# Performance work log

Measured on AMD Instinct MI355X. Metric: run time of the kernel, lower is better.

Reference implementation:

```python
import jax, jax.numpy as jnp
import numpy as np

C = 256; G = 16; GC = C // G; K = 3; P = K * K
N = 4; H = 64; W = 64
PAD = 1; OFFSET_SCALE = 1.0; LN_EPS = 1e-5


def setup_inputs() -> dict:
    key = jax.random.key(0)
    ks = jax.random.split(key, 8)
    s = 0.02
    return {
        "x": jax.random.normal(ks[0], (N, C, H, W), jnp.float32),
        "dw_w": jax.random.normal(ks[1], (C, 1, K, K), jnp.float32) * s,
        "dw_b": jnp.zeros((C,), jnp.float32),
        "ln_g": jnp.ones((C,), jnp.float32),
        "ln_b": jnp.zeros((C,), jnp.float32),
        "off_w": jax.random.normal(ks[2], (C, G * P * 2), jnp.float32) * s,
        "off_b": jnp.zeros((G * P * 2,), jnp.float32),
        "mask_w": jax.random.normal(ks[3], (C, G * P), jnp.float32) * s,
        "mask_b": jnp.zeros((G * P,), jnp.float32),
        "inp_w": jax.random.normal(ks[4], (C, C), jnp.float32) * s,
        "inp_b": jnp.zeros((C,), jnp.float32),
        "out_w": jax.random.normal(ks[5], (C, C), jnp.float32) * s,
        "out_b": jnp.zeros((C,), jnp.float32),
    }


def _dcnv3_nchw(x, dw_w, dw_b, ln_g, ln_b, off_w, off_b, mask_w, mask_b,
                inp_w, inp_b, out_w, out_b):
    # NCHW -> NHWC (wrapper permute)
    xn = jnp.transpose(x, (0, 2, 3, 1))                      # (N,H,W,C)
    x_proj = xn @ inp_w + inp_b                              # input_proj

    # offset/mask branch: depthwise conv (NCHW) -> LayerNorm (channels-last) -> GELU
    x1 = jax.lax.conv_general_dilated(
        x, dw_w, window_strides=(1, 1), padding=((PAD, PAD), (PAD, PAD)),
        dimension_numbers=("NCHW", "OIHW", "NCHW"), feature_group_count=C)
    x1 = jnp.transpose(x1, (0, 2, 3, 1)) + dw_b
    mu = x1.mean(-1, keepdims=True)
    var = ((x1 - mu) ** 2).mean(-1, keepdims=True)
    x1 = (x1 - mu) * jax.lax.rsqrt(var + LN_EPS) * ln_g + ln_b
    x1 = jax.nn.gelu(x1, approximate=False)

    offset = (x1 @ off_w + off_b).reshape(N, H, W, G, P, 2)  # (x,y) pairs
    mask = jax.nn.softmax((x1 @ mask_w + mask_b).reshape(N, H, W, G, P), axis=-1)

    # pad sampled feature map with zeros (F.pad before sampling)
    xp = jnp.pad(x_proj, ((0, 0), (PAD, PAD), (PAD, PAD), (0, 0)))
    Hin, Win = H + 2 * PAD, W + 2 * PAD
    xg = xp.reshape(N, Hin, Win, G, GC)

    # reference points, normalized by padded size
    ref_y = (jnp.arange(H, dtype=jnp.float32) + PAD + 0.5) / Hin
    ref_x = (jnp.arange(W, dtype=jnp.float32) + PAD + 0.5) / Win
    ref = jnp.stack([jnp.broadcast_to(ref_x[None, :], (H, W)),
                     jnp.broadcast_to(ref_y[:, None], (H, W))], -1)  # (H,W,2)

    # dilation grid: x varies in the outer loop (torch meshgrid 'ij')
    d = jnp.arange(K, dtype=jnp.float32) - (K - 1) // 2     # [-1,0,1]
    gx = jnp.repeat(d, K) / Win
    gy = jnp.tile(d, K) / Hin
    grid = jnp.stack([gx, gy], -1)                           # (P,2)

    norm = jnp.array([Win, Hin], jnp.float32)
    loc = (ref[None, :, :, None, None, :] + grid * OFFSET_SCALE
           + offset * OFFSET_SCALE / norm)                   # (N,H,W,G,P,2)

    # grid_sample bilinear, align_corners=False, zero padding
    px = loc[..., 0] * Win - 0.5
    py = loc[..., 1] * Hin - 0.5
    x0 = jnp.floor(px); y0 = jnp.floor(py)
    wx = px - x0; wy = py - y0
    x0i = x0.astype(jnp.int32); y0i = y0.astype(jnp.int32)

    n_idx = jnp.arange(N)[:, None, None, None, None]
    g_idx = jnp.arange(G)[None, None, None, :, None]

    def corner(iy, ix, w):
        valid = (iy >= 0) & (iy < Hin) & (ix >= 0) & (ix < Win)
        v = xg[n_idx, jnp.clip(iy, 0, Hin - 1), jnp.clip(ix, 0, Win - 1), g_idx]
        wgt = jnp.where(valid, w, 0.0) * mask                # fold mask into weights
        return jnp.einsum("nhwgp,nhwgpc->nhwgc", wgt, v)

    out = (corner(y0i, x0i, (1 - wy) * (1 - wx))
           + corner(y0i, x0i + 1, (1 - wy) * wx)
           + corner(y0i + 1, x0i, wy * (1 - wx))
           + corner(y0i + 1, x0i + 1, wy * wx))               # (N,H,W,G,GC)

    out = out.reshape(N, H, W, C) @ out_w + out_b            # output_proj
    return jnp.transpose(out, (0, 3, 1, 2))                  # NHWC -> NCHW


def reference(x, dw_w, dw_b, ln_g, ln_b, off_w, off_b, mask_w, mask_b,
              inp_w, inp_b, out_w, out_b):
    return _dcnv3_nchw(x, dw_w, dw_b, ln_g, ln_b, off_w, off_b,
                       mask_w, mask_b, inp_w, inp_b, out_w, out_b)
```

## Files before the change

### kernel.cpp

```cpp
#include <hip/hip_runtime.h>
#include <hip/hip_bf16.h>
#include <math.h>


using bf16x8 = __attribute__((ext_vector_type(8))) short;
using f32x4  = __attribute__((ext_vector_type(4))) float;

#define GLOBAL_AS __attribute__((address_space(1)))
#define LDS_AS    __attribute__((address_space(3)))

static __device__ inline void g2lds16(const void* g, void* l) {
  __builtin_amdgcn_global_load_lds((const GLOBAL_AS int*)g, (LDS_AS int*)l, 16, 0, 0);
}
static __device__ inline unsigned short f2bf(float v) {
  __hip_bfloat16 b = __float2bfloat16(v);
  return *reinterpret_cast<unsigned short*>(&b);
}
static __device__ inline float us2f(unsigned short u) {
  union { unsigned u; float f; } c; c.u = ((unsigned)u) << 16; return c.f;
}

__global__ __launch_bounds__(256) void prep_xt_k(
    const float* __restrict__ x,
    const float* __restrict__ inp_w, const float* __restrict__ off_w,
    const float* __restrict__ off_b, const float* __restrict__ mask_w,
    const float* __restrict__ mask_b, const float* __restrict__ out_w,
    __hip_bfloat16* __restrict__ BtI, __hip_bfloat16* __restrict__ BtOM,
    __hip_bfloat16* __restrict__ BtO, float* __restrict__ bOM,
    __hip_bfloat16* __restrict__ xT)
{
  __shared__ float tile[32][65];
  const int b = blockIdx.x, t = threadIdx.x;
  if (b < 1024) {
    if (b < 256) {
      int n = b;
      BtI[n * 256 + t] = __float2bfloat16(inp_w[t * 256 + n]);
    } else if (b < 768) {
      int n = b - 256;
      float v = 0.f;
      if (n < 288) v = off_w[t * 288 + n];
      else if (n < 432) v = mask_w[t * 144 + (n - 288)];
      BtOM[n * 256 + t] = __float2bfloat16(v);
      if (b == 256) {
        for (int idx = t; idx < 512; idx += 256) {
          float bv = (idx < 288) ? off_b[idx] : ((idx < 432) ? mask_b[idx - 288] : 0.f);
          bOM[idx] = bv;
        }
      }
    } else {
      int n = b - 768;
      BtO[n * 256 + t] = __float2bfloat16(out_w[t * 256 + n]);
    }
    return;
  }
  const int i = b - 1024;
  const int hw0 = (i & 63) * 64, c0 = ((i >> 6) & 7) * 32, n4 = i >> 9;
  #pragma unroll
  for (int r = 0; r < 8; ++r) {
    int idx = t + r * 256;
    int cl = idx >> 6, wl = idx & 63;
    tile[cl][wl] = x[(size_t)n4 * 1048576 + (size_t)(c0 + cl) * 4096 + hw0 + wl];
  }
  __syncthreads();
  #pragma unroll
  for (int r = 0; r < 2; ++r) {
    int idx = t + r * 256;
    int pixl = idx >> 3, cq = idx & 7;
    unsigned short b0 = f2bf(tile[cq * 4 + 0][pixl]);
    unsigned short b1 = f2bf(tile[cq * 4 + 1][pixl]);
    unsigned short b2 = f2bf(tile[cq * 4 + 2][pixl]);
    unsigned short b3 = f2bf(tile[cq * 4 + 3][pixl]);
    uint2 u;
    u.x = (unsigned)b0 | ((unsigned)b1 << 16);
    u.y = (unsigned)b2 | ((unsigned)b3 << 16);
    *(uint2*)&xT[((size_t)n4 * 4096 + hw0 + pixl) * 256 + c0 + cq * 4] = u;
  }
}

struct G64 {
  f32x4 acc[2][2];
  int wave, lane, quad, lr, wm, wn;
};

static __device__ inline void g64_loop(
    G64& g, const __hip_bfloat16* __restrict__ A,
    const __hip_bfloat16* __restrict__ Bt, size_t m0, int n0,
    short* As, short* Bs, int t)
{
  #pragma unroll
  for (int i = 0; i < 2; ++i)
    #pragma unroll
    for (int j = 0; j < 2; ++j)
      g.acc[i][j] = (f32x4){0.f, 0.f, 0.f, 0.f};
  const int row = t >> 2, kq = t & 3;
  for (int kt = 0; kt < 256; kt += 32) {
    g2lds16(A + (m0 + row) * 256 + kt + kq * 8, (char*)As + t * 16);
    g2lds16(Bt + (size_t)(n0 + row) * 256 + kt + kq * 8, (char*)Bs + t * 16);
    __syncthreads();
    bf16x8 bfv[2];
    #pragma unroll
    for (int ni = 0; ni < 2; ++ni)
      bfv[ni] = *(const bf16x8*)&Bs[(g.wn * 32 + ni * 16 + g.lr) * 32 + g.quad * 8];
    #pragma unroll
    for (int mi = 0; mi < 2; ++mi) {
      bf16x8 af = *(const bf16x8*)&As[(g.wm * 32 + mi * 16 + g.lr) * 32 + g.quad * 8];
      #pragma unroll
      for (int ni = 0; ni < 2; ++ni)
        g.acc[mi][ni] = __builtin_amdgcn_mfma_f32_16x16x32_bf16(af, bfv[ni], g.acc[mi][ni], 0, 0, 0);
    }
    __syncthreads();
  }
}

__global__ __launch_bounds__(256) void gemm_i(
    const __hip_bfloat16* __restrict__ xT, const __hip_bfloat16* __restrict__ BtI,
    const float* __restrict__ inp_b, __hip_bfloat16* __restrict__ xpu)
{
  __shared__ __align__(16) char smem[8192];
  short* As = (short*)smem;
  short* Bs = (short*)(smem + 4096);
  const int t = threadIdx.x;
  const int n0 = blockIdx.x * 64;
  const size_t m0 = (size_t)blockIdx.y * 64;

  G64 g;
  g.wave = t >> 6; g.lane = t & 63; g.quad = g.lane >> 4; g.lr = g.lane & 15;
  g.wm = g.wave >> 1; g.wn = g.wave & 1;
  g64_loop(g, xT, BtI, m0, n0, As, Bs, t);

  #pragma unroll
  for (int mi = 0; mi < 2; ++mi) {
    #pragma unroll
    for (int ni = 0; ni < 2; ++ni) {
      int col = n0 + g.wn * 32 + ni * 16 + g.lr;
      float bv = inp_b[col];
      #pragma unroll
      for (int reg = 0; reg < 4; ++reg) {
        size_t m = m0 + g.wm * 32 + mi * 16 + g.quad * 4 + reg;
        xpu[m * 256 + col] = __float2bfloat16(g.acc[mi][ni][reg] + bv);
      }
    }
  }
}

__global__ __launch_bounds__(1024) void stage2_k(
    const __hip_bfloat16* __restrict__ xT,
    const float* __restrict__ dw_w, const float* __restrict__ dw_b,
    const float* __restrict__ ln_g, const float* __restrict__ ln_b,
    const __hip_bfloat16* __restrict__ BtOM, const float* __restrict__ bOM,
    __hip_bfloat16* __restrict__ om)
{
  __shared__ __align__(16) char smem[62464];
  unsigned short* x1t = (unsigned short*)smem;
  unsigned short* xs  = (unsigned short*)(smem + 33792);
  float* wgt  = (float*)(smem + 33792 + 15360);
  float* psq  = (float*)(smem + 33792 + 15360 + 1152);
  float* murs = (float*)(smem + 33792 + 15360 + 1152 + 8192);
  short* Bs   = (short*)(smem + 33792);

  const int blk = blockIdx.x;
  const int n4 = blk >> 6, h = blk & 63;
  const int t = threadIdx.x;
  const int w = t & 63, q = t >> 6;

  float s1 = 0.f, s2 = 0.f;
  for (int chunk = 0; chunk < 8; ++chunk) {
    const int ch0 = chunk * 32;
    if (t < 768) {
      int r = t >> 8, i = t & 255;
      int px = i >> 2, cq = i & 3;
      int hh = h + r - 1;
      uint4 v = {0, 0, 0, 0};
      if ((unsigned)hh < 64u)
        v = *(const uint4*)(xT + ((size_t)n4 * 4096 + (size_t)hh * 64 + px) * 256 + ch0 + cq * 8);
      *(uint4*)&xs[(r * 64 + px) * 40 + cq * 8] = v;
    }
    if (t < 288) {
      int p = t >> 5, lc = t & 31;
      wgt[p * 32 + lc] = dw_w[(ch0 + lc) * 9 + p];
    }
    __syncthreads();
    {
      int c = ch0 + 2 * q;
      float a0 = dw_b[c], a1 = dw_b[c + 1];
      #pragma unroll
      for (int p = 0; p < 9; ++p) {
        int dh = p / 3, dwd = p % 3 - 1;
        int ww = w + dwd;
        if ((unsigned)ww < 64u) {
          unsigned xv = *(const unsigned*)&xs[(dh * 64 + ww) * 40 + 2 * q];
          float wa = wgt[p * 32 + 2 * q], wb = wgt[p * 32 + 2 * q + 1];
          a0 = fmaf(us2f((unsigned short)(xv & 0xffff)), wa, a0);
          a1 = fmaf(us2f((unsigned short)(xv >> 16)), wb, a1);
        }
      }
      s1 += a0 + a1;
      s2 = fmaf(a0, a0, fmaf(a1, a1, s2));
      unsigned pk = (unsigned)f2bf(a0) | ((unsigned)f2bf(a1) << 16);
      *(unsigned*)&x1t[w * 264 + c] = pk;
    }
    __syncthreads();
  }

  psq[q * 64 + w] = s1;
  psq[1024 + q * 64 + w] = s2;
  __syncthreads();
  if (t < 64) {
    float a = 0.f, b = 0.f;
    #pragma unroll
    for (int j = 0; j < 16; ++j) { a += psq[j * 64 + t]; b += psq[1024 + j * 64 + t]; }
    float mu = a * (1.f / 256.f);
    murs[t] = mu;
    murs[64 + t] = rsqrtf(b * (1.f / 256.f) - mu * mu + 1e-5f);
  }
  __syncthreads();
  {
    float mu = murs[w], rs = murs[64 + w];
    #pragma unroll
    for (int chunk = 0; chunk < 8; ++chunk) {
      int c = chunk * 32 + 2 * q;
      unsigned pk = *(const unsigned*)&x1t[w * 264 + c];
      float v0 = us2f((unsigned short)(pk & 0xffff));
      float v1 = us2f((unsigned short)(pk >> 16));
      float y0 = fmaf((v0 - mu) * rs, ln_g[c], ln_b[c]);
      float y1 = fmaf((v1 - mu) * rs, ln_g[c + 1], ln_b[c + 1]);
      float g0 = 0.5f * y0 * (1.f + erff(y0 * 0.70710678f));
      float g1 = 0.5f * y1 * (1.f + erff(y1 * 0.70710678f));
      *(unsigned*)&x1t[w * 264 + c] = (unsigned)f2bf(g0) | ((unsigned)f2bf(g1) << 16);
    }
  }
  __syncthreads();

  const int wave = t >> 6, lane = t & 63;
  const int quad = lane >> 4, lr = lane & 15;
  const int wm = wave >> 2, wn = wave & 3;
  f32x4 acc[7];
  #pragma unroll
  for (int i = 0; i < 7; ++i) acc[i] = (f32x4){0.f, 0.f, 0.f, 0.f};

  for (int kt = 0; kt < 256; kt += 32) {
    __syncthreads();
    {
      int col = t >> 2, kq = t & 3;
      g2lds16(BtOM + (size_t)col * 256 + kt + kq * 8, (char*)Bs + t * 16);
      int j = t + 1024;
      if (j < 1792) {
        col = j >> 2; kq = j & 3;
        g2lds16(BtOM + (size_t)col * 256 + kt + kq * 8, (char*)Bs + j * 16);
      }
    }
    __syncthreads();
    bf16x8 af = *(const bf16x8*)&x1t[(wm * 16 + lr) * 264 + kt + quad * 8];
    #pragma unroll
    for (int ni = 0; ni < 7; ++ni) {
      bf16x8 bf = *(const bf16x8*)&Bs[(wn * 112 + ni * 16 + lr) * 32 + quad * 8];
      acc[ni] = __builtin_amdgcn_mfma_f32_16x16x32_bf16(af, bf, acc[ni], 0, 0, 0);
    }
  }

  const size_t pix0 = (size_t)n4 * 4096 + (size_t)h * 64;
  #pragma unroll
  for (int ni = 0; ni < 7; ++ni) {
    int col = wn * 112 + ni * 16 + lr;
    if (col < 432) {
      float bv = bOM[col];
      #pragma unroll
      for (int reg = 0; reg < 4; ++reg) {
        int m = wm * 16 + quad * 4 + reg;
        om[(pix0 + m) * 448 + col] = __float2bfloat16(acc[ni][reg] + bv);
      }
    }
  }
}

__global__ __launch_bounds__(256) void sample_k(
    const __hip_bfloat16* __restrict__ xpu, const __hip_bfloat16* __restrict__ om,
    __hip_bfloat16* __restrict__ samp)
{
  __shared__ unsigned short oms[16 * 448];
  const int bid = blockIdx.x;
  const int region = bid & 7;
  const int q = bid >> 3;
  const int pix0 = region * 2048 + q * 16;
  const int t = threadIdx.x;

  {
    const uint4* gsrc = (const uint4*)(om + (size_t)pix0 * 448);
    uint4* ldst = (uint4*)oms;
    #pragma unroll
    for (int r = 0; r < 4; ++r) {
      int i = t + r * 256;
      if (i < 896) ldst[i] = gsrc[i];
    }
  }
  __syncthreads();

  const int g = t & 15;
  const int pl = t >> 4;
  const int pix = pix0 + pl;
  const int n4 = pix >> 12;
  const int hw = pix & 4095;
  const int h = hw >> 6, w = hw & 63;

  float mk[9];
  {
    const unsigned short* mp = &oms[pl * 448 + 288 + g * 9];
    float mx = -1e30f;
    #pragma unroll
    for (int p = 0; p < 9; ++p) { mk[p] = us2f(mp[p]); mx = fmaxf(mx, mk[p]); }
    float se = 0.f;
    #pragma unroll
    for (int p = 0; p < 9; ++p) { mk[p] = __expf(mk[p] - mx); se += mk[p]; }
    float inv = 1.f / se;
    #pragma unroll
    for (int p = 0; p < 9; ++p) mk[p] *= inv;
  }

  const unsigned short* op = &oms[pl * 448 + g * 18];
  const __hip_bfloat16* xpg = xpu + (g << 4);
  float ax[16];
  #pragma unroll
  for (int i = 0; i < 16; ++i) ax[i] = 0.f;

  auto corner = [&](int iy, int ix, float wt) {
    if ((unsigned)(iy - 1) >= 64u || (unsigned)(ix - 1) >= 64u) return;
    const __hip_bfloat16* src =
        xpg + ((size_t)((n4 << 12) + (iy - 1) * 64 + (ix - 1)) << 8);
    uint4 u0 = *(const uint4*)src;
    uint4 u1 = *(const uint4*)(src + 8);
    const unsigned uu[8] = {u0.x, u0.y, u0.z, u0.w, u1.x, u1.y, u1.z, u1.w};
    #pragma unroll
    for (int i = 0; i < 8; ++i) {
      float lo = us2f((unsigned short)(uu[i] & 0xffff));
      float hi = us2f((unsigned short)(uu[i] >> 16));
      ax[2 * i + 0] = fmaf(wt, lo, ax[2 * i + 0]);
      ax[2 * i + 1] = fmaf(wt, hi, ax[2 * i + 1]);
    }
  };

  #pragma unroll
  for (int p = 0; p < 9; ++p) {
    float ox = us2f(op[2 * p]), oy = us2f(op[2 * p + 1]);
    float px = (float)(w + p / 3) + ox;
    float py = (float)(h + p % 3) + oy;
    float xf = floorf(px), yf = floorf(py);
    float wx = px - xf, wy = py - yf;
    int ix = (int)xf, iy = (int)yf;
    float m = mk[p];
    corner(iy,     ix,     (1.f - wy) * (1.f - wx) * m);
    corner(iy,     ix + 1, (1.f - wy) * wx * m);
    corner(iy + 1, ix,     wy * (1.f - wx) * m);
    corner(iy + 1, ix + 1, wy * wx * m);
  }

  unsigned short ub[16];
  #pragma unroll
  for (int i = 0; i < 16; ++i) ub[i] = f2bf(ax[i]);
  uint4* d4 = (uint4*)(samp + (size_t)pix * 256 + (g << 4));
  uint4 u0, u1;
  u0.x = (unsigned)ub[0] | ((unsigned)ub[1] << 16);
  u0.y = (unsigned)ub[2] | ((unsigned)ub[3] << 16);
  u0.z = (unsigned)ub[4] | ((unsigned)ub[5] << 16);
  u0.w = (unsigned)ub[6] | ((unsigned)ub[7] << 16);
  u1.x = (unsigned)ub[8] | ((unsigned)ub[9] << 16);
  u1.y = (unsigned)ub[10] | ((unsigned)ub[11] << 16);
  u1.z = (unsigned)ub[12] | ((unsigned)ub[13] << 16);
  u1.w = (unsigned)ub[14] | ((unsigned)ub[15] << 16);
  d4[0] = u0; d4[1] = u1;
}

__global__ __launch_bounds__(256) void gemm_o(
    const __hip_bfloat16* __restrict__ samp, const __hip_bfloat16* __restrict__ BtO,
    const float* __restrict__ out_b, float* __restrict__ out)
{
  __shared__ __align__(16) char smem[8448];
  short* As = (short*)smem;
  short* Bs = (short*)(smem + 4096);
  float* tb = (float*)smem;
  const int t = threadIdx.x;
  const int n0 = blockIdx.x * 64;
  const size_t m0 = (size_t)blockIdx.y * 64;

  G64 g;
  g.wave = t >> 6; g.lane = t & 63; g.quad = g.lane >> 4; g.lr = g.lane & 15;
  g.wm = g.wave >> 1; g.wn = g.wave & 1;
  g64_loop(g, samp, BtO, m0, n0, As, Bs, t);

  const int n4 = (int)(m0 >> 12), hw0 = (int)(m0 & 4095);
  for (int qc = 0; qc < 2; ++qc) {
    __syncthreads();
    if (g.wn == qc) {
      #pragma unroll
      for (int ni = 0; ni < 2; ++ni) {
        int cl = ni * 16 + g.lr;
        float bv = out_b[n0 + qc * 32 + cl];
        #pragma unroll
        for (int mi = 0; mi < 2; ++mi)
          #pragma unroll
          for (int reg = 0; reg < 4; ++reg)
            tb[cl * 65 + g.wm * 32 + mi * 16 + g.quad * 4 + reg] =
                g.acc[mi][ni][reg] + bv;
      }
    }
    __syncthreads();
    #pragma unroll
    for (int r = 0; r < 2; ++r) {
      int idx = t + r * 256;
      int row = idx >> 4, mc = (idx & 15) * 4;
      int co = n0 + qc * 32 + row;
      float4 v;
      v.x = tb[row * 65 + mc + 0];
      v.y = tb[row * 65 + mc + 1];
      v.z = tb[row * 65 + mc + 2];
      v.w = tb[row * 65 + mc + 3];
      *(float4*)&out[(size_t)(n4 * 256 + co) * 4096 + hw0 + mc] = v;
    }
  }
}

extern "C" void kernel_launch(void* const* d_in, const int* in_sizes, int n_in,
                              void* d_out, int out_size, void* d_ws, size_t ws_size,
                              hipStream_t stream) {
  const float* x      = (const float*)d_in[0];
  const float* dw_w   = (const float*)d_in[1];
  const float* dw_b   = (const float*)d_in[2];
  const float* ln_g   = (const float*)d_in[3];
  const float* ln_b   = (const float*)d_in[4];
  const float* off_w  = (const float*)d_in[5];
  const float* off_b  = (const float*)d_in[6];
  const float* mask_w = (const float*)d_in[7];
  const float* mask_b = (const float*)d_in[8];
  const float* inp_w  = (const float*)d_in[9];
  const float* inp_b  = (const float*)d_in[10];
  const float* out_w  = (const float*)d_in[11];
  const float* out_b  = (const float*)d_in[12];
  float* out = (float*)d_out;

  char* w0 = (char*)d_ws;
  __hip_bfloat16* xpu  = (__hip_bfloat16*)(w0);
  __hip_bfloat16* xT   = (__hip_bfloat16*)(w0 + 8388608);
  __hip_bfloat16* samp = xT;
  __hip_bfloat16* om   = (__hip_bfloat16*)(w0 + 16777216);
  __hip_bfloat16* BtI  = (__hip_bfloat16*)(w0 + 31457280);
  __hip_bfloat16* BtOM = (__hip_bfloat16*)(w0 + 31588352);
  __hip_bfloat16* BtO  = (__hip_bfloat16*)(w0 + 31850496);
  float*          bOM  = (float*)(w0 + 31981568);
  if (ws_size < 31983616) return;

  prep_xt_k<<<3072, 256, 0, stream>>>(x, inp_w, off_w, off_b, mask_w, mask_b,
                                      out_w, BtI, BtOM, BtO, bOM, xT);
  gemm_i<<<dim3(4, 256), 256, 0, stream>>>(xT, BtI, inp_b, xpu);
  stage2_k<<<256, 1024, 0, stream>>>(xT, dw_w, dw_b, ln_g, ln_b, BtOM, bOM, om);
  sample_k<<<1024, 256, 0, stream>>>(xpu, om, samp);
  gemm_o<<<dim3(4, 256), 256, 0, stream>>>(samp, BtO, out_b, out);
}
```

Before: 163.1 us.

## Merge input GEMM into stage2 launch and fuse sampling with output projection

Runs the input-projection GEMM as extra blocks (four 256-thread sub-tiles per 1024-thread block) inside the stage2 launch so the two independent branches share one grid. Sampling and the output GEMM become one kernel: each block samples 64 pixels into an LDS tile and feeds it straight into MFMA against the output weights, so the sampled bf16 buffer never goes through global memory. Block indices are swizzled across regions. This cuts two launches and a full intermediate round trip, at the cost of big 1024-thread blocks with heavy LDS use, and of reading offsets and masks directly from global memory.

```diff
diff --git a/kernel.cpp b/kernel.cpp
--- a/kernel.cpp
+++ b/kernel.cpp
@@ -79,7 +79,7 @@
 
 struct G64 {
   f32x4 acc[2][2];
-  int wave, lane, quad, lr, wm, wn;
+  int lane, quad, lr, wm, wn;
 };
 
 static __device__ inline void g64_loop(
@@ -112,45 +112,49 @@
   }
 }
 
-__global__ __launch_bounds__(256) void gemm_i(
-    const __hip_bfloat16* __restrict__ xT, const __hip_bfloat16* __restrict__ BtI,
-    const float* __restrict__ inp_b, __hip_bfloat16* __restrict__ xpu)
-{
-  __shared__ __align__(16) char smem[8192];
-  short* As = (short*)smem;
-  short* Bs = (short*)(smem + 4096);
-  const int t = threadIdx.x;
-  const int n0 = blockIdx.x * 64;
-  const size_t m0 = (size_t)blockIdx.y * 64;
-
-  G64 g;
-  g.wave = t >> 6; g.lane = t & 63; g.quad = g.lane >> 4; g.lr = g.lane & 15;
-  g.wm = g.wave >> 1; g.wn = g.wave & 1;
-  g64_loop(g, xT, BtI, m0, n0, As, Bs, t);
-
-  #pragma unroll
-  for (int mi = 0; mi < 2; ++mi) {
-    #pragma unroll
-    for (int ni = 0; ni < 2; ++ni) {
-      int col = n0 + g.wn * 32 + ni * 16 + g.lr;
-      float bv = inp_b[col];
-      #pragma unroll
-      for (int reg = 0; reg < 4; ++reg) {
-        size_t m = m0 + g.wm * 32 + mi * 16 + g.quad * 4 + reg;
-        xpu[m * 256 + col] = __float2bfloat16(g.acc[mi][ni][reg] + bv);
-      }
-    }
-  }
-}
-
-__global__ __launch_bounds__(1024) void stage2_k(
+__global__ __launch_bounds__(1024) void stage2_gi_k(
     const __hip_bfloat16* __restrict__ xT,
     const float* __restrict__ dw_w, const float* __restrict__ dw_b,
     const float* __restrict__ ln_g, const float* __restrict__ ln_b,
     const __hip_bfloat16* __restrict__ BtOM, const float* __restrict__ bOM,
-    __hip_bfloat16* __restrict__ om)
+    __hip_bfloat16* __restrict__ om,
+    const __hip_bfloat16* __restrict__ BtI, const float* __restrict__ inp_b,
+    __hip_bfloat16* __restrict__ xpu)
 {
   __shared__ __align__(16) char smem[62464];
+  const int bid = blockIdx.x;
+
+  if (bid >= 256) {
+    const int sb = threadIdx.x >> 8;
+    const int t = threadIdx.x & 255;
+    const int tile = (bid - 256) * 4 + sb;
+    const int n0 = (tile & 3) * 64;
+    const size_t m0 = (size_t)(tile >> 2) * 64;
+    short* As = (short*)(smem + sb * 8192);
+    short* Bs = (short*)(smem + sb * 8192 + 4096);
+
+    G64 g;
+    g.lane = t & 63; g.quad = g.lane >> 4; g.lr = g.lane & 15;
+    int wave = t >> 6;
+    g.wm = wave >> 1; g.wn = wave & 1;
+    g64_loop(g, xT, BtI, m0, n0, As, Bs, t);
+
+    #pragma unroll
+    for (int mi = 0; mi < 2; ++mi) {
+      #pragma unroll
+      for (int ni = 0; ni < 2; ++ni) {
+        int col = n0 + g.wn * 32 + ni * 16 + g.lr;
+        float bv = inp_b[col];
+        #pragma unroll
+        for (int reg = 0; reg < 4; ++reg) {
+          size_t m = m0 + g.wm * 32 + mi * 16 + g.quad * 4 + reg;
+          xpu[m * 256 + col] = __float2bfloat16(g.acc[mi][ni][reg] + bv);
+        }
+      }
+    }
+    return;
+  }
+
   unsigned short* x1t = (unsigned short*)smem;
   unsigned short* xs  = (unsigned short*)(smem + 33792);
   float* wgt  = (float*)(smem + 33792 + 15360);
@@ -158,7 +162,7 @@
   float* murs = (float*)(smem + 33792 + 15360 + 1152 + 8192);
   short* Bs   = (short*)(smem + 33792);
 
-  const int blk = blockIdx.x;
+  const int blk = ((bid & 7) << 5) | (bid >> 3);
   const int n4 = blk >> 6, h = blk & 63;
   const int t = threadIdx.x;
   const int w = t & 63, q = t >> 6;
@@ -273,148 +277,124 @@
   }
 }
 
-__global__ __launch_bounds__(256) void sample_k(
+__global__ __launch_bounds__(1024) void fused_so_k(
     const __hip_bfloat16* __restrict__ xpu, const __hip_bfloat16* __restrict__ om,
-    __hip_bfloat16* __restrict__ samp)
+    const __hip_bfloat16* __restrict__ BtO, const float* __restrict__ out_b,
+    float* __restrict__ out)
 {
-  __shared__ unsigned short oms[16 * 448];
+  __shared__ __align__(16) char smem[50176];
+  unsigned short* st = (unsigned short*)smem;
+  short* Bs = (short*)(smem + 33792);
+
   const int bid = blockIdx.x;
-  const int region = bid & 7;
-  const int q = bid >> 3;
-  const int pix0 = region * 2048 + q * 16;
+  const int swz = ((bid & 7) << 5) | (bid >> 3);
+  const int pix0 = swz << 6;
   const int t = threadIdx.x;
 
   {
-    const uint4* gsrc = (const uint4*)(om + (size_t)pix0 * 448);
-    uint4* ldst = (uint4*)oms;
-    #pragma unroll
-    for (int r = 0; r < 4; ++r) {
-      int i = t + r * 256;
-      if (i < 896) ldst[i] = gsrc[i];
-    }
-  }
-  __syncthreads();
-
-  const int g = t & 15;
-  const int pl = t >> 4;
-  const int pix = pix0 + pl;
-  const int n4 = pix >> 12;
-  const int hw = pix & 4095;
-  const int h = hw >> 6, w = hw & 63;
-
-  float mk[9];
-  {
-    const unsigned short* mp = &oms[pl * 448 + 288 + g * 9];
-    float mx = -1e30f;
-    #pragma unroll
-    for (int p = 0; p < 9; ++p) { mk[p] = us2f(mp[p]); mx = fmaxf(mx, mk[p]); }
-    float se = 0.f;
-    #pragma unroll
-    for (int p = 0; p < 9; ++p) { mk[p] = __expf(mk[p] - mx); se += mk[p]; }
-    float inv = 1.f / se;
-    #pragma unroll
-    for (int p = 0; p < 9; ++p) mk[p] *= inv;
-  }
-
-  const unsigned short* op = &oms[pl * 448 + g * 18];
-  const __hip_bfloat16* xpg = xpu + (g << 4);
-  float ax[16];
-  #pragma unroll
-  for (int i = 0; i < 16; ++i) ax[i] = 0.f;
-
-  auto corner = [&](int iy, int ix, float wt) {
-    if ((unsigned)(iy - 1) >= 64u || (unsigned)(ix - 1) >= 64u) return;
-    const __hip_bfloat16* src =
-        xpg + ((size_t)((n4 << 12) + (iy - 1) * 64 + (ix - 1)) << 8);
-    uint4 u0 = *(const uint4*)src;
-    uint4 u1 = *(const uint4*)(src + 8);
-    const unsigned uu[8] = {u0.x, u0.y, u0.z, u0.w, u1.x, u1.y, u1.z, u1.w};
-    #pragma unroll
-    for (int i = 0; i < 8; ++i) {
-      float lo = us2f((unsigned short)(uu[i] & 0xffff));
-      float hi = us2f((unsigned short)(uu[i] >> 16));
-      ax[2 * i + 0] = fmaf(wt, lo, ax[2 * i + 0]);
-      ax[2 * i + 1] = fmaf(wt, hi, ax[2 * i + 1]);
-    }
-  };
-
-  #pragma unroll
-  for (int p = 0; p < 9; ++p) {
-    float ox = us2f(op[2 * p]), oy = us2f(op[2 * p + 1]);
-    float px = (float)(w + p / 3) + ox;
-    float py = (float)(h + p % 3) + oy;
-    float xf = floorf(px), yf = floorf(py);
-    float wx = px - xf, wy = py - yf;
-    int ix = (int)xf, iy = (int)yf;
-    float m = mk[p];
-    corner(iy,     ix,     (1.f - wy) * (1.f - wx) * m);
-    corner(iy,     ix + 1, (1.f - wy) * wx * m);
-    corner(iy + 1, ix,     wy * (1.f - wx) * m);
-    corner(iy + 1, ix + 1, wy * wx * m);
-  }
-
-  unsigned short ub[16];
-  #pragma unroll
-  for (int i = 0; i < 16; ++i) ub[i] = f2bf(ax[i]);
-  uint4* d4 = (uint4*)(samp + (size_t)pix * 256 + (g << 4));
-  uint4 u0, u1;
-  u0.x = (unsigned)ub[0] | ((unsigned)ub[1] << 16);
-  u0.y = (unsigned)ub[2] | ((unsigned)ub[3] << 16);
-  u0.z = (unsigned)ub[4] | ((unsigned)ub[5] << 16);
-  u0.w = (unsigned)ub[6] | ((unsigned)ub[7] << 16);
-  u1.x = (unsigned)ub[8] | ((unsigned)ub[9] << 16);
-  u1.y = (unsigned)ub[10] | ((unsigned)ub[11] << 16);
-  u1.z = (unsigned)ub[12] | ((unsigned)ub[13] << 16);
-  u1.w = (unsigned)ub[14] | ((unsigned)ub[15] << 16);
-  d4[0] = u0; d4[1] = u1;
-}
-
-__global__ __launch_bounds__(256) void gemm_o(
-    const __hip_bfloat16* __restrict__ samp, const __hip_bfloat16* __restrict__ BtO,
-    const float* __restrict__ out_b, float* __restrict__ out)
-{
-  __shared__ __align__(16) char smem[8448];
-  short* As = (short*)smem;
-  short* Bs = (short*)(smem + 4096);
-  float* tb = (float*)smem;
-  const int t = threadIdx.x;
-  const int n0 = blockIdx.x * 64;
-  const size_t m0 = (size_t)blockIdx.y * 64;
-
-  G64 g;
-  g.wave = t >> 6; g.lane = t & 63; g.quad = g.lane >> 4; g.lr = g.lane & 15;
-  g.wm = g.wave >> 1; g.wn = g.wave & 1;
-  g64_loop(g, samp, BtO, m0, n0, As, Bs, t);
-
-  const int n4 = (int)(m0 >> 12), hw0 = (int)(m0 & 4095);
-  for (int qc = 0; qc < 2; ++qc) {
-    __syncthreads();
-    if (g.wn == qc) {
-      #pragma unroll
-      for (int ni = 0; ni < 2; ++ni) {
-        int cl = ni * 16 + g.lr;
-        float bv = out_b[n0 + qc * 32 + cl];
-        #pragma unroll
-        for (int mi = 0; mi < 2; ++mi)
-          #pragma unroll
-          for (int reg = 0; reg < 4; ++reg)
-            tb[cl * 65 + g.wm * 32 + mi * 16 + g.quad * 4 + reg] =
-                g.acc[mi][ni][reg] + bv;
-      }
-    }
-    __syncthreads();
-    #pragma unroll
-    for (int r = 0; r < 2; ++r) {
-      int idx = t + r * 256;
-      int row = idx >> 4, mc = (idx & 15) * 4;
-      int co = n0 + qc * 32 + row;
-      float4 v;
-      v.x = tb[row * 65 + mc + 0];
-      v.y = tb[row * 65 + mc + 1];
-      v.z = tb[row * 65 + mc + 2];
-      v.w = tb[row * 65 + mc + 3];
-      *(float4*)&out[(size_t)(n4 * 256 + co) * 4096 + hw0 + mc] = v;
-    }
+    const int pl = t >> 4, g = t & 15;
+    const int pix = pix0 + pl;
+    const int n4s = pix >> 12;
+    const int hw = pix & 4095;
+    const int h = hw >> 6, w = hw & 63;
+    const unsigned short* omp = (const unsigned short*)om + (size_t)pix * 448;
+
+    float mk[9];
+    {
+      float mx = -1e30f;
+      #pragma unroll
+      for (int p = 0; p < 9; ++p) { mk[p] = us2f(omp[288 + g * 9 + p]); mx = fmaxf(mx, mk[p]); }
+      float se = 0.f;
+      #pragma unroll
+      for (int p = 0; p < 9; ++p) { mk[p] = __expf(mk[p] - mx); se += mk[p]; }
+      float inv = 1.f / se;
+      #pragma unroll
+      for (int p = 0; p < 9; ++p) mk[p] *= inv;
+    }
+
+    const __hip_bfloat16* xpg = xpu + (g << 4);
+    float ax[16];
+    #pragma unroll
+    for (int i = 0; i < 16; ++i) ax[i] = 0.f;
+
+    auto corner = [&](int iy, int ix, float wt) {
+      if ((unsigned)(iy - 1) >= 64u || (unsigned)(ix - 1) >= 64u) return;
+      const __hip_bfloat16* src =
+          xpg + ((size_t)((n4s << 12) + (iy - 1) * 64 + (ix - 1)) << 8);
+      uint4 u0 = *(const uint4*)src;
+      uint4 u1 = *(const uint4*)(src + 8);
+      const unsigned uu[8] = {u0.x, u0.y, u0.z, u0.w, u1.x, u1.y, u1.z, u1.w};
+      #pragma unroll
+      for (int i = 0; i < 8; ++i) {
+        float lo = us2f((unsigned short)(uu[i] & 0xffff));
+        float hi = us2f((unsigned short)(uu[i] >> 16));
+        ax[2 * i + 0] = fmaf(wt, lo, ax[2 * i + 0]);
+        ax[2 * i + 1] = fmaf(wt, hi, ax[2 * i + 1]);
+      }
+    };
+
+    #pragma unroll
+    for (int p = 0; p < 9; ++p) {
+      float ox = us2f(omp[g * 18 + 2 * p]), oy = us2f(omp[g * 18 + 2 * p + 1]);
+      float px = (float)(w + p / 3) + ox;
+      float py = (float)(h + p % 3) + oy;
+      float xf = floorf(px), yf = floorf(py);
+      float wx = px - xf, wy = py - yf;
+      int ix = (int)xf, iy = (int)yf;
+      float m = mk[p];
+      corner(iy,     ix,     (1.f - wy) * (1.f - wx) * m);
+      corner(iy,     ix + 1, (1.f - wy) * wx * m);
+      corner(iy + 1, ix,     wy * (1.f - wx) * m);
+      corner(iy + 1, ix + 1, wy * wx * m);
+    }
+
+    unsigned short ub[16];
+    #pragma unroll
+    for (int i = 0; i < 16; ++i) ub[i] = f2bf(ax[i]);
+    uint4 u0, u1;
+    u0.x = (unsigned)ub[0] | ((unsigned)ub[1] << 16);
+    u0.y = (unsigned)ub[2] | ((unsigned)ub[3] << 16);
+    u0.z = (unsigned)ub[4] | ((unsigned)ub[5] << 16);
+    u0.w = (unsigned)ub[6] | ((unsigned)ub[7] << 16);
+    u1.x = (unsigned)ub[8] | ((unsigned)ub[9] << 16);
+    u1.y = (unsigned)ub[10] | ((unsigned)ub[11] << 16);
+    u1.z = (unsigned)ub[12] | ((unsigned)ub[13] << 16);
+    u1.w = (unsigned)ub[14] | ((unsigned)ub[15] << 16);
+    *(uint4*)&st[pl * 264 + g * 16] = u0;
+    *(uint4*)&st[pl * 264 + g * 16 + 8] = u1;
+  }
+
+  const int wave = t >> 6, lane = t & 63;
+  const int quad = lane >> 4, lr = lane & 15;
+  const int wm = wave >> 2, wn = wave & 3;
+  f32x4 acc[4];
+  #pragma unroll
+  for (int i = 0; i < 4; ++i) acc[i] = (f32x4){0.f, 0.f, 0.f, 0.f};
+
+  for (int kt = 0; kt < 256; kt += 32) {
+    __syncthreads();
+    {
+      int col = t >> 2, kq = t & 3;
+      g2lds16(BtO + (size_t)col * 256 + kt + kq * 8, (char*)Bs + t * 16);
+    }
+    __syncthreads();
+    bf16x8 af = *(const bf16x8*)&st[(wm * 16 + lr) * 264 + kt + quad * 8];
+    #pragma unroll
+    for (int ni = 0; ni < 4; ++ni) {
+      bf16x8 bf = *(const bf16x8*)&Bs[(wn * 64 + ni * 16 + lr) * 32 + quad * 8];
+      acc[ni] = __builtin_amdgcn_mfma_f32_16x16x32_bf16(af, bf, acc[ni], 0, 0, 0);
+    }
+  }
+
+  const int n4 = pix0 >> 12, hw0 = pix0 & 4095;
+  #pragma unroll
+  for (int ni = 0; ni < 4; ++ni) {
+    int col = wn * 64 + ni * 16 + lr;
+    float bv = out_b[col];
+    float4 v;
+    v.x = acc[ni][0] + bv; v.y = acc[ni][1] + bv;
+    v.z = acc[ni][2] + bv; v.w = acc[ni][3] + bv;
+    *(float4*)&out[(size_t)(n4 * 256 + col) * 4096 + hw0 + wm * 16 + quad * 4] = v;
   }
 }
 
@@ -439,7 +419,6 @@
   char* w0 = (char*)d_ws;
   __hip_bfloat16* xpu  = (__hip_bfloat16*)(w0);
   __hip_bfloat16* xT   = (__hip_bfloat16*)(w0 + 8388608);
-  __hip_bfloat16* samp = xT;
   __hip_bfloat16* om   = (__hip_bfloat16*)(w0 + 16777216);
   __hip_bfloat16* BtI  = (__hip_bfloat16*)(w0 + 31457280);
   __hip_bfloat16* BtOM = (__hip_bfloat16*)(w0 + 31588352);
@@ -449,8 +428,7 @@
 
   prep_xt_k<<<3072, 256, 0, stream>>>(x, inp_w, off_w, off_b, mask_w, mask_b,
                                       out_w, BtI, BtOM, BtO, bOM, xT);
-  gemm_i<<<dim3(4, 256), 256, 0, stream>>>(xT, BtI, inp_b, xpu);
-  stage2_k<<<256, 1024, 0, stream>>>(xT, dw_w, dw_b, ln_g, ln_b, BtOM, bOM, om);
-  sample_k<<<1024, 256, 0, stream>>>(xpu, om, samp);
-  gemm_o<<<dim3(4, 256), 256, 0, stream>>>(samp, BtO, out_b, out);
-}
+  stage2_gi_k<<<512, 1024, 0, stream>>>(xT, dw_w, dw_b, ln_g, ln_b, BtOM, bOM, om,
+                                        BtI, inp_b, xpu);
+  fused_so_k<<<256, 1024, 0, stream>>>(xpu, om, BtO, out_b, out);
+}
```

Result: no change. 161.4 us (-1.1%).
